# Kernel optimization log

Measured on AMD Instinct MI355X. Metric: run time of the kernel, lower is better.

The kernel has to match this reference:

```python
import jax, jax.numpy as jnp
import numpy as np

N = 100000   # vertices
E = 600000   # directed edges
F = 200000   # triangle faces
CIN = 128
COUT = 128
H = 32       # metric MLP hidden
D = 3        # embedding_dim (3D metric)
TRI = D * (D + 1) // 2  # 6 params of a symmetric 3x3


def setup_inputs() -> dict:
    key = jax.random.key(0)
    ks = jax.random.split(key, 8)
    features = jax.random.normal(ks[0], (N, CIN), jnp.float32)
    vertices = jax.random.normal(ks[1], (N, 3), jnp.float32)
    edges = jax.random.randint(ks[2], (2, E), 0, N)
    faces = jax.random.randint(ks[3], (3, F), 0, N)
    # metric MLP params (edge tangent vector -> symmetric metric params)
    W1 = jax.random.normal(ks[4], (D, H), jnp.float32) / np.sqrt(D)
    b1 = jnp.zeros((H,), jnp.float32)
    W2 = jax.random.normal(ks[5], (H, TRI), jnp.float32) / np.sqrt(H)
    b2 = jnp.zeros((TRI,), jnp.float32)
    # per-vertex feature transform
    Wlin = jax.random.normal(ks[6], (CIN, COUT), jnp.float32) / np.sqrt(CIN)
    blin = jnp.zeros((COUT,), jnp.float32)
    return dict(features=features, vertices=vertices, edges=edges, faces=faces,
                W1=W1, b1=b1, W2=W2, b2=b2, Wlin=Wlin, blin=blin)


def _vertex_normals(vertices, faces):
    # area-weighted vertex normals from triangle faces
    v0, v1, v2 = vertices[faces[0]], vertices[faces[1]], vertices[faces[2]]
    fn = jnp.cross(v1 - v0, v2 - v0)                       # [F,3]
    n = jnp.zeros_like(vertices)
    n = n.at[faces[0]].add(fn).at[faces[1]].add(fn).at[faces[2]].add(fn)
    return n / (jnp.linalg.norm(n, axis=-1, keepdims=True) + 1e-8)


def _sym_from_flat(theta):
    # theta [E,6] -> symmetric [E,3,3]
    iu0, iu1 = jnp.triu_indices(D)
    S = jnp.zeros((theta.shape[0], D, D), theta.dtype)
    S = S.at[:, iu0, iu1].set(theta)
    S = S.at[:, iu1, iu0].set(theta)
    return S


def reference(features, vertices, edges, faces, W1, b1, W2, b2, Wlin, blin):
    eps = 1e-5
    src, dst = edges[0], edges[1]
    normals = _vertex_normals(vertices, faces)             # [N,3] ('tangent' info)
    d = vertices[dst] - vertices[src]                      # [E,3] edge vectors
    n_src = normals[src]
    t = d - jnp.sum(d * n_src, -1, keepdims=True) * n_src  # tangent-plane projection
    # learned metric per edge: MLP -> symmetric S, PSD metric M = S S
    h = jax.nn.relu(t @ W1 + b1)                           # [E,H]
    theta = h @ W2 + b2                                    # [E,6]
    S = _sym_from_flat(theta)                              # [E,3,3]
    M = jnp.einsum('eij,ejk->eik', S, S)                   # PSD metric
    q = jnp.einsum('ei,eij,ej->e', t, M, t)                # metric quadratic form
    w = jnp.exp(-q)                                        # positive edge weights
    # per-vertex linear, then metric-weighted mean aggregation over in-edges
    x = features @ Wlin + blin                             # [N,COUT]
    num = jax.ops.segment_sum(w[:, None] * x[src], dst, num_segments=N)
    den = jax.ops.segment_sum(w, dst, num_segments=N) + eps
    out = num / den[:, None]                               # MetricConv output
    # MetricConvBlock: manual per-feature normalization + ELU
    mu = out.mean(axis=0)
    sd = out.std(axis=0, ddof=1)                           # torch std is unbiased
    out = (out - mu) / (sd + eps)
    return jax.nn.elu(out)
```

## Files before the change

kernel.cpp:

```cpp
#include <hip/hip_runtime.h>
#include <hip/hip_bf16.h>
#include <math.h>

#define N_V 100000
#define N_E 600000
#define N_F 200000

typedef __attribute__((ext_vector_type(8))) short bf16x8;
typedef __attribute__((ext_vector_type(4))) float f32x4;

#define FUSED_BLOCKS 1563
#define FACE_BLOCKS 782
#define EDGE_BLOCKS 2344
#define PACK_BLOCKS 64

__device__ __forceinline__ unsigned short f2bf(float f) {
    unsigned int u = __builtin_bit_cast(unsigned int, f);
    u += 0x7fffu + ((u >> 16) & 1u);
    return (unsigned short)(u >> 16);
}

__global__ void k_fn(const float* __restrict__ vtx, const int* __restrict__ faces,
                     const float* __restrict__ Wlin,
                     float4* __restrict__ fnbuf4,
                     int* __restrict__ head_f, int* __restrict__ next_f,
                     unsigned short* __restrict__ Wb) {
    int b = blockIdx.x;
    int t = threadIdx.x;
    if (b < FACE_BLOCKS) {
        int f = b * 256 + t;
        if (f >= N_F) return;
        int i0 = faces[f], i1 = faces[N_F + f], i2 = faces[2 * N_F + f];
        #pragma unroll
        for (int j = 0; j < 3; j++) {
            int v = (j == 0) ? i0 : (j == 1 ? i1 : i2);
            int c = 3 * f + j;
            int old = atomicExch(&head_f[v], c);
            next_f[c] = old;
        }
        float ax = vtx[3 * i0], ay = vtx[3 * i0 + 1], az = vtx[3 * i0 + 2];
        float bx = vtx[3 * i1] - ax, by = vtx[3 * i1 + 1] - ay, bz = vtx[3 * i1 + 2] - az;
        float cx = vtx[3 * i2] - ax, cy = vtx[3 * i2 + 1] - ay, cz = vtx[3 * i2 + 2] - az;
        float4 fn;
        fn.x = by * cz - bz * cy;
        fn.y = bz * cx - bx * cz;
        fn.z = bx * cy - by * cx;
        fn.w = 0.f;
        fnbuf4[f] = fn;
    } else {
        int i = (b - FACE_BLOCKS) * 256 + t;
        int j = i & 7;
        int lane = (i >> 3) & 63;
        int ct = (i >> 9) & 7;
        int kk = i >> 12;
        int k = kk * 32 + (lane >> 4) * 8 + j;
        int n = ct * 16 + (lane & 15);
        Wb[i] = f2bf(Wlin[k * 128 + n]);
    }
}

__global__ void k_vnorm(const float4* __restrict__ fnbuf4,
                        const int* __restrict__ head_f, const int* __restrict__ next_f,
                        float* __restrict__ nrm) {
    int v = blockIdx.x * 256 + threadIdx.x;
    if (v >= N_V) return;
    float nx = 0.f, ny = 0.f, nz = 0.f;
    int c = head_f[v];
    while (c >= 0) {
        float4 fn = fnbuf4[(unsigned)c / 3u];
        nx += fn.x; ny += fn.y; nz += fn.z;
        c = next_f[c];
    }
    float inv = 1.f / (sqrtf(nx * nx + ny * ny + nz * nz) + 1e-8f);
    nrm[3 * v] = nx * inv; nrm[3 * v + 1] = ny * inv; nrm[3 * v + 2] = nz * inv;
}

__global__ void k_edge(const float* __restrict__ vtx, const int* __restrict__ edges,
                       const float* __restrict__ nrm,
                       const float* __restrict__ W1, const float* __restrict__ b1,
                       const float* __restrict__ W2, const float* __restrict__ b2,
                       int* __restrict__ head_e, uint2* __restrict__ enode) {
    __shared__ float sW1[96], sb1[32], sW2[192], sb2[6];
    int t = threadIdx.x;
    if (t < 96)  sW1[t] = W1[t];
    if (t < 32)  sb1[t] = b1[t];
    if (t < 192) sW2[t] = W2[t];
    if (t < 6)   sb2[t] = b2[t];
    __syncthreads();
    int e = blockIdx.x * blockDim.x + t;
    if (e >= N_E) return;
    int s = edges[e], d = edges[N_E + e];
    int old = atomicExch(&head_e[d], e);
    float dx = vtx[3 * d] - vtx[3 * s];
    float dy = vtx[3 * d + 1] - vtx[3 * s + 1];
    float dz = vtx[3 * d + 2] - vtx[3 * s + 2];
    float nx = nrm[3 * s], ny = nrm[3 * s + 1], nz = nrm[3 * s + 2];
    float dp = dx * nx + dy * ny + dz * nz;
    float tx = dx - dp * nx, ty = dy - dp * ny, tz = dz - dp * nz;
    float th0 = sb2[0], th1 = sb2[1], th2 = sb2[2], th3 = sb2[3], th4 = sb2[4], th5 = sb2[5];
    #pragma unroll
    for (int j = 0; j < 32; j++) {
        float h = tx * sW1[j] + ty * sW1[32 + j] + tz * sW1[64 + j] + sb1[j];
        h = fmaxf(h, 0.f);
        const float* w2r = &sW2[j * 6];
        th0 += h * w2r[0]; th1 += h * w2r[1]; th2 += h * w2r[2];
        th3 += h * w2r[3]; th4 += h * w2r[4]; th5 += h * w2r[5];
    }
    float ux = th0 * tx + th1 * ty + th2 * tz;
    float uy = th1 * tx + th3 * ty + th4 * tz;
    float uz = th2 * tx + th4 * ty + th5 * tz;
    float q = ux * ux + uy * uy + uz * uz;
    float w = expf(-q);
    unsigned int w16 = f2bf(w);
    uint2 nd;
    nd.x = (unsigned int)(old + 1) | ((w16 & 0xFFFu) << 20);
    nd.y = (unsigned int)s | ((w16 >> 12) << 17);
    enode[e] = nd;
}

__global__ __launch_bounds__(512) void k_fused(const float* __restrict__ feat,
                                               const int* __restrict__ head_e,
                                               const uint2* __restrict__ enode,
                                               const unsigned short* __restrict__ Wb,
                                               const float* __restrict__ blin,
                                               float* __restrict__ out,
                                               float* __restrict__ partials) {
    __shared__ __align__(16) unsigned short At[64 * 136];
    __shared__ float gs[64];
    int t = threadIdx.x;
    int hw = t >> 5;
    int hl = t & 31;
    int vb = blockIdx.x * 64 + hw * 4;

    float4 a0 = {0,0,0,0}, a1 = {0,0,0,0}, a2 = {0,0,0,0}, a3 = {0,0,0,0};
    float d0 = 0.f, d1 = 0.f, d2 = 0.f, d3 = 0.f;
    int e0 = (vb + 0 < N_V) ? head_e[vb + 0] : -1;
    int e1 = (vb + 1 < N_V) ? head_e[vb + 1] : -1;
    int e2 = (vb + 2 < N_V) ? head_e[vb + 2] : -1;
    int e3 = (vb + 3 < N_V) ? head_e[vb + 3] : -1;

    while ((e0 >= 0) || (e1 >= 0) || (e2 >= 0) || (e3 >= 0)) {
        if (e0 >= 0) {
            uint2 nd = enode[e0];
            unsigned int wb = (nd.x >> 20) | (((nd.y >> 17) & 0xFu) << 12);
            float w = __builtin_bit_cast(float, wb << 16);
            const float4 f = *(const float4*)(feat + (size_t)(nd.y & 0x1FFFFu) * 128 + 4 * hl);
            a0.x += w * f.x; a0.y += w * f.y; a0.z += w * f.z; a0.w += w * f.w;
            d0 += w;
            e0 = (int)(nd.x & 0xFFFFFu) - 1;
        }
        if (e1 >= 0) {
            uint2 nd = enode[e1];
            unsigned int wb = (nd.x >> 20) | (((nd.y >> 17) & 0xFu) << 12);
            float w = __builtin_bit_cast(float, wb << 16);
            const float4 f = *(const float4*)(feat + (size_t)(nd.y & 0x1FFFFu) * 128 + 4 * hl);
            a1.x += w * f.x; a1.y += w * f.y; a1.z += w * f.z; a1.w += w * f.w;
            d1 += w;
            e1 = (int)(nd.x & 0xFFFFFu) - 1;
        }
        if (e2 >= 0) {
            uint2 nd = enode[e2];
            unsigned int wb = (nd.x >> 20) | (((nd.y >> 17) & 0xFu) << 12);
            float w = __builtin_bit_cast(float, wb << 16);
            const float4 f = *(const float4*)(feat + (size_t)(nd.y & 0x1FFFFu) * 128 + 4 * hl);
            a2.x += w * f.x; a2.y += w * f.y; a2.z += w * f.z; a2.w += w * f.w;
            d2 += w;
            e2 = (int)(nd.x & 0xFFFFFu) - 1;
        }
        if (e3 >= 0) {
            uint2 nd = enode[e3];
            unsigned int wb = (nd.x >> 20) | (((nd.y >> 17) & 0xFu) << 12);
            float w = __builtin_bit_cast(float, wb << 16);
            const float4 f = *(const float4*)(feat + (size_t)(nd.y & 0x1FFFFu) * 128 + 4 * hl);
            a3.x += w * f.x; a3.y += w * f.y; a3.z += w * f.z; a3.w += w * f.w;
            d3 += w;
            e3 = (int)(nd.x & 0xFFFFFu) - 1;
        }
    }
    #pragma unroll
    for (int j = 0; j < 4; j++) {
        float4 a = (j == 0) ? a0 : (j == 1) ? a1 : (j == 2) ? a2 : a3;
        float dn = (j == 0) ? d0 : (j == 1) ? d1 : (j == 2) ? d2 : d3;
        float inv = 1.f / (dn + 1e-5f);
        ushort4 p;
        p.x = f2bf(a.x * inv); p.y = f2bf(a.y * inv);
        p.z = f2bf(a.z * inv); p.w = f2bf(a.w * inv);
        int row = hw * 4 + j;
        *(ushort4*)(&At[row * 136 + 4 * hl]) = p;
        if (hl == 0) gs[row] = dn * inv;
    }
    __syncthreads();

    int ct = t >> 6;
    int lane = t & 63;
    int m = lane & 15, quad = lane >> 4;
    bf16x8 bfr[4];
    #pragma unroll
    for (int kk = 0; kk < 4; kk++)
        bfr[kk] = *(const bf16x8*)(Wb + (((kk * 8 + ct) * 64 + lane) << 3));
    float bl = blin[ct * 16 + m];
    float ssr = 0.f, qqr = 0.f;
    #pragma unroll
    for (int tile = 0; tile < 4; tile++) {
        f32x4 acc = (f32x4){0.f, 0.f, 0.f, 0.f};
        #pragma unroll
        for (int kk = 0; kk < 4; kk++) {
            bf16x8 af = *(const bf16x8*)(&At[(tile * 16 + m) * 136 + kk * 32 + quad * 8]);
            acc = __builtin_amdgcn_mfma_f32_16x16x32_bf16(af, bfr[kk], acc, 0, 0, 0);
        }
        int r0 = blockIdx.x * 64 + tile * 16;
        #pragma unroll
        for (int reg = 0; reg < 4; reg++) {
            int r = r0 + quad * 4 + reg;
            float g = gs[tile * 16 + quad * 4 + reg];
            float val = acc[reg] + bl * g;
            if (r < N_V) out[(size_t)r * 128 + ct * 16 + m] = val;
            ssr += val; qqr += val * val;
        }
    }
    ssr += __shfl_xor(ssr, 16); qqr += __shfl_xor(qqr, 16);
    ssr += __shfl_xor(ssr, 32); qqr += __shfl_xor(qqr, 32);
    if (quad == 0) {
        partials[(size_t)blockIdx.x * 256 + ct * 16 + m] = ssr;
        partials[(size_t)blockIdx.x * 256 + 128 + ct * 16 + m] = qqr;
    }
}

__global__ __launch_bounds__(64) void k_rstats(const float* __restrict__ partials,
                                               float* __restrict__ stats) {
    int c = blockIdx.x;
    int lane = threadIdx.x;
    float s = 0.f, q = 0.f;
    for (int b = lane; b < FUSED_BLOCKS; b += 64) {
        s += partials[(size_t)b * 256 + c];
        q += partials[(size_t)b * 256 + 128 + c];
    }
    #pragma unroll
    for (int off = 32; off; off >>= 1) {
        s += __shfl_down(s, off);
        q += __shfl_down(q, off);
    }
    if (lane == 0) {
        float mu = s * (1.f / N_V);
        float var = (q - s * mu) * (1.f / (N_V - 1));
        float sd = sqrtf(fmaxf(var, 0.f));
        stats[c] = mu;
        stats[128 + c] = 1.f / (sd + 1e-5f);
    }
}

__global__ void k_finalize(float* __restrict__ out, const float* __restrict__ stats) {
    int i = blockIdx.x * blockDim.x + threadIdx.x;
    if (i >= N_V * 32) return;
    float4 v = ((float4*)out)[i];
    int c0 = (i * 4) & 127;
    float mu0 = stats[c0], mu1 = stats[c0 + 1], mu2 = stats[c0 + 2], mu3 = stats[c0 + 3];
    float is0 = stats[128 + c0], is1 = stats[128 + c0 + 1], is2 = stats[128 + c0 + 2], is3 = stats[128 + c0 + 3];
    v.x = (v.x - mu0) * is0; v.y = (v.y - mu1) * is1;
    v.z = (v.z - mu2) * is2; v.w = (v.w - mu3) * is3;
    v.x = v.x > 0.f ? v.x : expm1f(v.x);
    v.y = v.y > 0.f ? v.y : expm1f(v.y);
    v.z = v.z > 0.f ? v.z : expm1f(v.z);
    v.w = v.w > 0.f ? v.w : expm1f(v.w);
    ((float4*)out)[i] = v;
}

extern "C" void kernel_launch(void* const* d_in, const int* in_sizes, int n_in,
                              void* d_out, int out_size, void* d_ws, size_t ws_size,
                              hipStream_t stream) {
    const float* feat  = (const float*)d_in[0];
    const float* vtx   = (const float*)d_in[1];
    const int*   edges = (const int*)d_in[2];
    const int*   faces = (const int*)d_in[3];
    const float* W1   = (const float*)d_in[4];
    const float* b1   = (const float*)d_in[5];
    const float* W2   = (const float*)d_in[6];
    const float* b2   = (const float*)d_in[7];
    const float* Wlin = (const float*)d_in[8];
    const float* blin = (const float*)d_in[9];
    float* out = (float*)d_out;

    float* ws = (float*)d_ws;
    int*   head_e   = (int*)ws;
    float* nrm3     = ws + 100000;
    float* partials = ws + 100000;
    int*   head_f   = (int*)(ws + 500128);
    int*   next_f   = (int*)(ws + 600128);
    float4* fnbuf4  = (float4*)(ws + 1200128);
    uint2* enode    = (uint2*)(ws + 500128);
    unsigned short* Wb = (unsigned short*)(ws + 2000128);
    float* stats    = ws;

    hipMemsetAsync(head_e, 0xFF, 100000 * sizeof(int), stream);
    hipMemsetAsync(head_f, 0xFF, 100000 * sizeof(int), stream);

    k_fn<<<FACE_BLOCKS + PACK_BLOCKS, 256, 0, stream>>>(vtx, faces, Wlin, fnbuf4,
                                                        head_f, next_f, Wb);
    k_vnorm<<<(N_V + 255) / 256, 256, 0, stream>>>(fnbuf4, head_f, next_f, nrm3);
    k_edge<<<EDGE_BLOCKS, 256, 0, stream>>>(vtx, edges, nrm3, W1, b1, W2, b2,
                                            head_e, enode);
    k_fused<<<FUSED_BLOCKS, 512, 0, stream>>>(feat, head_e, enode, Wb, blin,
                                              out, partials);
    k_rstats<<<128, 64, 0, stream>>>(partials, stats);
    k_finalize<<<(N_V * 32 + 255) / 256, 256, 0, stream>>>(out, stats);
}
```

Before: 277.4 us.

## Scatter face normals with atomics and widen fused aggregation tile to 128 rows

Vertex normals are now accumulated by float atomicAdd directly from the face kernel, and normalization moves into the edge kernel. This removes the linked-list build, the k_vnorm pass and one memset. Separately, the fused gather/GEMM kernel now handles 128 vertices per block, with 16 lanes per vertex each loading two float4s, so it launches half as many blocks. The atomics introduce contention and make normal summation order nondeterministic. Normalization is now recomputed for every edge, and the larger tile uses more shared memory and registers.

```diff
diff --git a/kernel.cpp b/kernel.cpp
--- a/kernel.cpp
+++ b/kernel.cpp
@@ -9,7 +9,7 @@
 typedef __attribute__((ext_vector_type(8))) short bf16x8;
 typedef __attribute__((ext_vector_type(4))) float f32x4;
 
-#define FUSED_BLOCKS 1563
+#define FUSED_BLOCKS 782
 #define FACE_BLOCKS 782
 #define EDGE_BLOCKS 2344
 #define PACK_BLOCKS 64
@@ -22,8 +22,7 @@
 
 __global__ void k_fn(const float* __restrict__ vtx, const int* __restrict__ faces,
                      const float* __restrict__ Wlin,
-                     float4* __restrict__ fnbuf4,
-                     int* __restrict__ head_f, int* __restrict__ next_f,
+                     float* __restrict__ nrm,
                      unsigned short* __restrict__ Wb) {
     int b = blockIdx.x;
     int t = threadIdx.x;
@@ -31,22 +30,21 @@
         int f = b * 256 + t;
         if (f >= N_F) return;
         int i0 = faces[f], i1 = faces[N_F + f], i2 = faces[2 * N_F + f];
-        #pragma unroll
-        for (int j = 0; j < 3; j++) {
-            int v = (j == 0) ? i0 : (j == 1 ? i1 : i2);
-            int c = 3 * f + j;
-            int old = atomicExch(&head_f[v], c);
-            next_f[c] = old;
-        }
         float ax = vtx[3 * i0], ay = vtx[3 * i0 + 1], az = vtx[3 * i0 + 2];
         float bx = vtx[3 * i1] - ax, by = vtx[3 * i1 + 1] - ay, bz = vtx[3 * i1 + 2] - az;
         float cx = vtx[3 * i2] - ax, cy = vtx[3 * i2 + 1] - ay, cz = vtx[3 * i2 + 2] - az;
-        float4 fn;
-        fn.x = by * cz - bz * cy;
-        fn.y = bz * cx - bx * cz;
-        fn.z = bx * cy - by * cx;
-        fn.w = 0.f;
-        fnbuf4[f] = fn;
+        float fx = by * cz - bz * cy;
+        float fy = bz * cx - bx * cz;
+        float fz = bx * cy - by * cx;
+        atomicAdd(&nrm[3 * i0],     fx);
+        atomicAdd(&nrm[3 * i0 + 1], fy);
+        atomicAdd(&nrm[3 * i0 + 2], fz);
+        atomicAdd(&nrm[3 * i1],     fx);
+        atomicAdd(&nrm[3 * i1 + 1], fy);
+        atomicAdd(&nrm[3 * i1 + 2], fz);
+        atomicAdd(&nrm[3 * i2],     fx);
+        atomicAdd(&nrm[3 * i2 + 1], fy);
+        atomicAdd(&nrm[3 * i2 + 2], fz);
     } else {
         int i = (b - FACE_BLOCKS) * 256 + t;
         int j = i & 7;
@@ -57,22 +55,6 @@
         int n = ct * 16 + (lane & 15);
         Wb[i] = f2bf(Wlin[k * 128 + n]);
     }
-}
-
-__global__ void k_vnorm(const float4* __restrict__ fnbuf4,
-                        const int* __restrict__ head_f, const int* __restrict__ next_f,
-                        float* __restrict__ nrm) {
-    int v = blockIdx.x * 256 + threadIdx.x;
-    if (v >= N_V) return;
-    float nx = 0.f, ny = 0.f, nz = 0.f;
-    int c = head_f[v];
-    while (c >= 0) {
-        float4 fn = fnbuf4[(unsigned)c / 3u];
-        nx += fn.x; ny += fn.y; nz += fn.z;
-        c = next_f[c];
-    }
-    float inv = 1.f / (sqrtf(nx * nx + ny * ny + nz * nz) + 1e-8f);
-    nrm[3 * v] = nx * inv; nrm[3 * v + 1] = ny * inv; nrm[3 * v + 2] = nz * inv;
 }
 
 __global__ void k_edge(const float* __restrict__ vtx, const int* __restrict__ edges,
@@ -94,7 +76,9 @@
     float dx = vtx[3 * d] - vtx[3 * s];
     float dy = vtx[3 * d + 1] - vtx[3 * s + 1];
     float dz = vtx[3 * d + 2] - vtx[3 * s + 2];
-    float nx = nrm[3 * s], ny = nrm[3 * s + 1], nz = nrm[3 * s + 2];
+    float rx = nrm[3 * s], ry = nrm[3 * s + 1], rz = nrm[3 * s + 2];
+    float ninv = 1.f / (sqrtf(rx * rx + ry * ry + rz * rz) + 1e-8f);
+    float nx = rx * ninv, ny = ry * ninv, nz = rz * ninv;
     float dp = dx * nx + dy * ny + dz * nz;
     float tx = dx - dp * nx, ty = dy - dp * ny, tz = dz - dp * nz;
     float th0 = sb2[0], th1 = sb2[1], th2 = sb2[2], th3 = sb2[3], th4 = sb2[4], th5 = sb2[5];
@@ -125,14 +109,17 @@
                                                const float* __restrict__ blin,
                                                float* __restrict__ out,
                                                float* __restrict__ partials) {
-    __shared__ __align__(16) unsigned short At[64 * 136];
-    __shared__ float gs[64];
+    __shared__ __align__(16) unsigned short At[128 * 136];
+    __shared__ float gs[128];
     int t = threadIdx.x;
-    int hw = t >> 5;
-    int hl = t & 31;
-    int vb = blockIdx.x * 64 + hw * 4;
-
-    float4 a0 = {0,0,0,0}, a1 = {0,0,0,0}, a2 = {0,0,0,0}, a3 = {0,0,0,0};
+    int g = t >> 4;
+    int gl = t & 15;
+    int vb = blockIdx.x * 128 + g * 4;
+
+    float4 a0l = {0,0,0,0}, a0h = {0,0,0,0};
+    float4 a1l = {0,0,0,0}, a1h = {0,0,0,0};
+    float4 a2l = {0,0,0,0}, a2h = {0,0,0,0};
+    float4 a3l = {0,0,0,0}, a3h = {0,0,0,0};
     float d0 = 0.f, d1 = 0.f, d2 = 0.f, d3 = 0.f;
     int e0 = (vb + 0 < N_V) ? head_e[vb + 0] : -1;
     int e1 = (vb + 1 < N_V) ? head_e[vb + 1] : -1;
@@ -144,8 +131,10 @@
             uint2 nd = enode[e0];
             unsigned int wb = (nd.x >> 20) | (((nd.y >> 17) & 0xFu) << 12);
             float w = __builtin_bit_cast(float, wb << 16);
-            const float4 f = *(const float4*)(feat + (size_t)(nd.y & 0x1FFFFu) * 128 + 4 * hl);
-            a0.x += w * f.x; a0.y += w * f.y; a0.z += w * f.z; a0.w += w * f.w;
+            const float4* fp = (const float4*)(feat + (size_t)(nd.y & 0x1FFFFu) * 128 + 8 * gl);
+            float4 f0 = fp[0], f1 = fp[1];
+            a0l.x += w * f0.x; a0l.y += w * f0.y; a0l.z += w * f0.z; a0l.w += w * f0.w;
+            a0h.x += w * f1.x; a0h.y += w * f1.y; a0h.z += w * f1.z; a0h.w += w * f1.w;
             d0 += w;
             e0 = (int)(nd.x & 0xFFFFFu) - 1;
         }
@@ -153,8 +142,10 @@
             uint2 nd = enode[e1];
             unsigned int wb = (nd.x >> 20) | (((nd.y >> 17) & 0xFu) << 12);
             float w = __builtin_bit_cast(float, wb << 16);
-            const float4 f = *(const float4*)(feat + (size_t)(nd.y & 0x1FFFFu) * 128 + 4 * hl);
-            a1.x += w * f.x; a1.y += w * f.y; a1.z += w * f.z; a1.w += w * f.w;
+            const float4* fp = (const float4*)(feat + (size_t)(nd.y & 0x1FFFFu) * 128 + 8 * gl);
+            float4 f0 = fp[0], f1 = fp[1];
+            a1l.x += w * f0.x; a1l.y += w * f0.y; a1l.z += w * f0.z; a1l.w += w * f0.w;
+            a1h.x += w * f1.x; a1h.y += w * f1.y; a1h.z += w * f1.z; a1h.w += w * f1.w;
             d1 += w;
             e1 = (int)(nd.x & 0xFFFFFu) - 1;
         }
@@ -162,8 +153,10 @@
             uint2 nd = enode[e2];
             unsigned int wb = (nd.x >> 20) | (((nd.y >> 17) & 0xFu) << 12);
             float w = __builtin_bit_cast(float, wb << 16);
-            const float4 f = *(const float4*)(feat + (size_t)(nd.y & 0x1FFFFu) * 128 + 4 * hl);
-            a2.x += w * f.x; a2.y += w * f.y; a2.z += w * f.z; a2.w += w * f.w;
+            const float4* fp = (const float4*)(feat + (size_t)(nd.y & 0x1FFFFu) * 128 + 8 * gl);
+            float4 f0 = fp[0], f1 = fp[1];
+            a2l.x += w * f0.x; a2l.y += w * f0.y; a2l.z += w * f0.z; a2l.w += w * f0.w;
+            a2h.x += w * f1.x; a2h.y += w * f1.y; a2h.z += w * f1.z; a2h.w += w * f1.w;
             d2 += w;
             e2 = (int)(nd.x & 0xFFFFFu) - 1;
         }
@@ -171,23 +164,29 @@
             uint2 nd = enode[e3];
             unsigned int wb = (nd.x >> 20) | (((nd.y >> 17) & 0xFu) << 12);
             float w = __builtin_bit_cast(float, wb << 16);
-            const float4 f = *(const float4*)(feat + (size_t)(nd.y & 0x1FFFFu) * 128 + 4 * hl);
-            a3.x += w * f.x; a3.y += w * f.y; a3.z += w * f.z; a3.w += w * f.w;
+            const float4* fp = (const float4*)(feat + (size_t)(nd.y & 0x1FFFFu) * 128 + 8 * gl);
+            float4 f0 = fp[0], f1 = fp[1];
+            a3l.x += w * f0.x; a3l.y += w * f0.y; a3l.z += w * f0.z; a3l.w += w * f0.w;
+            a3h.x += w * f1.x; a3h.y += w * f1.y; a3h.z += w * f1.z; a3h.w += w * f1.w;
             d3 += w;
             e3 = (int)(nd.x & 0xFFFFFu) - 1;
         }
     }
     #pragma unroll
     for (int j = 0; j < 4; j++) {
-        float4 a = (j == 0) ? a0 : (j == 1) ? a1 : (j == 2) ? a2 : a3;
+        float4 al = (j == 0) ? a0l : (j == 1) ? a1l : (j == 2) ? a2l : a3l;
+        float4 ah = (j == 0) ? a0h : (j == 1) ? a1h : (j == 2) ? a2h : a3h;
         float dn = (j == 0) ? d0 : (j == 1) ? d1 : (j == 2) ? d2 : d3;
         float inv = 1.f / (dn + 1e-5f);
-        ushort4 p;
-        p.x = f2bf(a.x * inv); p.y = f2bf(a.y * inv);
-        p.z = f2bf(a.z * inv); p.w = f2bf(a.w * inv);
-        int row = hw * 4 + j;
-        *(ushort4*)(&At[row * 136 + 4 * hl]) = p;
-        if (hl == 0) gs[row] = dn * inv;
+        ushort4 p0, p1;
+        p0.x = f2bf(al.x * inv); p0.y = f2bf(al.y * inv);
+        p0.z = f2bf(al.z * inv); p0.w = f2bf(al.w * inv);
+        p1.x = f2bf(ah.x * inv); p1.y = f2bf(ah.y * inv);
+        p1.z = f2bf(ah.z * inv); p1.w = f2bf(ah.w * inv);
+        int row = g * 4 + j;
+        *(ushort4*)(&At[row * 136 + 8 * gl]) = p0;
+        *(ushort4*)(&At[row * 136 + 8 * gl + 4]) = p1;
+        if (gl == 0) gs[row] = dn * inv;
     }
     __syncthreads();
 
@@ -201,19 +200,19 @@
     float bl = blin[ct * 16 + m];
     float ssr = 0.f, qqr = 0.f;
     #pragma unroll
-    for (int tile = 0; tile < 4; tile++) {
+    for (int tile = 0; tile < 8; tile++) {
         f32x4 acc = (f32x4){0.f, 0.f, 0.f, 0.f};
         #pragma unroll
         for (int kk = 0; kk < 4; kk++) {
             bf16x8 af = *(const bf16x8*)(&At[(tile * 16 + m) * 136 + kk * 32 + quad * 8]);
             acc = __builtin_amdgcn_mfma_f32_16x16x32_bf16(af, bfr[kk], acc, 0, 0, 0);
         }
-        int r0 = blockIdx.x * 64 + tile * 16;
+        int r0 = blockIdx.x * 128 + tile * 16;
         #pragma unroll
         for (int reg = 0; reg < 4; reg++) {
             int r = r0 + quad * 4 + reg;
-            float g = gs[tile * 16 + quad * 4 + reg];
-            float val = acc[reg] + bl * g;
+            float g2 = gs[tile * 16 + quad * 4 + reg];
+            float val = acc[reg] + bl * g2;
             if (r < N_V) out[(size_t)r * 128 + ct * 16 + m] = val;
             ssr += val; qqr += val * val;
         }
@@ -284,19 +283,14 @@
     int*   head_e   = (int*)ws;
     float* nrm3     = ws + 100000;
     float* partials = ws + 100000;
-    int*   head_f   = (int*)(ws + 500128);
-    int*   next_f   = (int*)(ws + 600128);
-    float4* fnbuf4  = (float4*)(ws + 1200128);
     uint2* enode    = (uint2*)(ws + 500128);
     unsigned short* Wb = (unsigned short*)(ws + 2000128);
     float* stats    = ws;
 
     hipMemsetAsync(head_e, 0xFF, 100000 * sizeof(int), stream);
-    hipMemsetAsync(head_f, 0xFF, 100000 * sizeof(int), stream);
-
-    k_fn<<<FACE_BLOCKS + PACK_BLOCKS, 256, 0, stream>>>(vtx, faces, Wlin, fnbuf4,
-                                                        head_f, next_f, Wb);
-    k_vnorm<<<(N_V + 255) / 256, 256, 0, stream>>>(fnbuf4, head_f, next_f, nrm3);
+    hipMemsetAsync(nrm3, 0, 300000 * sizeof(float), stream);
+
+    k_fn<<<FACE_BLOCKS + PACK_BLOCKS, 256, 0, stream>>>(vtx, faces, Wlin, nrm3, Wb);
     k_edge<<<EDGE_BLOCKS, 256, 0, stream>>>(vtx, edges, nrm3, W1, b1, W2, b2,
                                             head_e, enode);
     k_fused<<<FUSED_BLOCKS, 512, 0, stream>>>(feat, head_e, enode, Wb, blin,
```

New measurement: 317.5 us. 1.14x slower.
